# Kernel tuning notes

Measured on AMD Instinct MI355X. Metric: run time of the kernel, lower is better.

Reference implementation:

```python
import jax, jax.numpy as jnp
import numpy as np
import math

# ---- physical constants (QMAV) ----
MASS = 1.5
GRAV = 9.81
_J_NP = np.diag([0.0211, 0.0219, 0.0366]).astype(np.float32)
J = jnp.asarray(_J_NP)
J_INV = jnp.asarray(np.linalg.inv(_J_NP).astype(np.float32))
KD_X = KD_Y = KD_Z = 0.10   # linear drag coeffs
K_H = 0.01                   # horizontal-velocity lift coeff
O_MIN, O_MAX = 0.0, 1000.0   # rotor speed limits [rad/s]
KT, KM, ARM = 1.0e-5, 1.0e-7, 0.15
_G_VEC = jnp.array([0.0, 0.0, GRAV], jnp.float32).reshape(1, 3, 1)  # NED, down positive


def make_G1():
    # [T, Mx, My, Mz] = G_1 @ [o1^2, o2^2, o3^2, o4^2], X-configuration mixer
    c = ARM * KT * math.sqrt(2.0) / 2.0
    return np.array([
        [KT,  KT,  KT,  KT],
        [-c,   c,   c,  -c],
        [-c,  -c,   c,   c],
        [-KM,  KM, -KM,  KM],
    ], dtype=np.float32)


def quat_to_rot(q):
    # q: [B,4,1] = (ew,ex,ey,ez) -> body-to-inertial rotation [B,3,3]
    ew, ex, ey, ez = q[:, 0, 0], q[:, 1, 0], q[:, 2, 0], q[:, 3, 0]
    r = jnp.stack([
        ew**2 + ex**2 - ey**2 - ez**2, 2*(ex*ey - ew*ez), 2*(ex*ez + ew*ey),
        2*(ex*ey + ew*ez), ew**2 - ex**2 + ey**2 - ez**2, 2*(ey*ez - ew*ex),
        2*(ex*ez - ew*ey), 2*(ey*ez + ew*ex), ew**2 - ex**2 - ey**2 + ez**2,
    ], axis=-1)
    return r.reshape(-1, 3, 3)


def quat_to_euler(q):
    ew, ex, ey, ez = q[:, 0:1, :], q[:, 1:2, :], q[:, 2:3, :], q[:, 3:4, :]
    phi = jnp.arctan2(2*(ew*ex + ey*ez), ew**2 + ez**2 - ex**2 - ey**2)
    theta = jnp.arcsin(jnp.clip(2*(ew*ey - ex*ez), -1.0, 1.0))
    psi = jnp.arctan2(2*(ew*ez + ex*ey), ew**2 + ex**2 - ey**2 - ez**2)
    return phi, theta, psi


def rigid_body_deriv(x, u):
    # x: [B,13,1] = [pos(3), v_world(3), quat(4), omega(3)]; u: [B,6,1] = [f_inertial(3), moment_body(3)]
    v = x[:, 3:6, :]
    q = x[:, 6:10, :]
    w = x[:, 10:13, :]
    f_i = u[:, 0:3, :]
    m_b = u[:, 3:6, :]
    pos_dot = v
    v_dot = f_i / MASS + _G_VEC
    ew, ex, ey, ez = q[:, 0:1, :], q[:, 1:2, :], q[:, 2:3, :], q[:, 3:4, :]
    p, qq, r = w[:, 0:1, :], w[:, 1:2, :], w[:, 2:3, :]
    q_dot = 0.5 * jnp.concatenate([
        -ex*p - ey*qq - ez*r,
         ew*p + ey*r - ez*qq,
         ew*qq - ex*r + ez*p,
         ew*r + ex*qq - ey*p,
    ], axis=1)
    Jw = jnp.einsum('ij,bjk->bik', J, w)
    w_dot = jnp.einsum('ij,bjk->bik', J_INV, m_b - jnp.cross(w, Jw, axis=1))
    return jnp.concatenate([pos_dot, v_dot, q_dot, w_dot], axis=1)


def rk4_step(x, u, dt):
    k1 = rigid_body_deriv(x, u)
    k2 = rigid_body_deriv(x + 0.5 * dt * k1, u)
    k3 = rigid_body_deriv(x + 0.5 * dt * k2, u)
    k4 = rigid_body_deriv(x + dt * k3, u)
    return x + (dt / 6.0) * (k1 + 2*k2 + 2*k3 + k4)


def setup_inputs() -> dict:
    key = jax.random.key(0)
    k1, k2 = jax.random.split(key)
    B = 1 << 20
    state = jax.random.normal(k1, (B, 32, 1), dtype=jnp.float32)
    # normalize the quaternion slice so the initial attitude is valid
    q = state[:, 9:13, :]
    state = state.at[:, 9:13, :].set(q / jnp.sqrt(jnp.sum(q**2, axis=1, keepdims=True)))
    delta = jax.random.uniform(k2, (B, 4, 1), dtype=jnp.float32) * O_MAX
    G_1 = jnp.asarray(make_G1())
    return {"state": state, "delta": delta, "G_1": G_1, "dt": 0.02}


def reference(state, delta, G_1, dt):
    # ---- forces / moments + wind-related state ----
    d = jnp.clip(delta, O_MIN, O_MAX)
    tt = jnp.einsum('ij,bjk->bik', G_1, d**2)  # [B,4,1] = [T, Mx, My, Mz]
    T = tt[:, 0:1, :]; Mx = tt[:, 1:2, :]; My = tt[:, 2:3, :]; Mz = tt[:, 3:4, :]
    R = quat_to_rot(state[:, 9:13, :])
    V_wind_b = jnp.einsum('bji,bjk->bik', R, state[:, 28:31, :])  # R^T @ wind_inertial
    u_r = state[:, 16:17, :] - V_wind_b[:, 0:1, :]
    v_r = state[:, 17:18, :] - V_wind_b[:, 1:2, :]
    w_r = state[:, 18:19, :] - V_wind_b[:, 2:3, :]
    Va = jnp.sqrt(u_r**2 + v_r**2 + w_r**2)
    u_safe = jnp.where(u_r == 0.0, 1.0, u_r)
    alpha = jnp.where(u_r == 0.0, math.pi / 2, jnp.arctan2(w_r, u_safe))
    Va_safe = jnp.where(Va == 0.0, 1.0, Va)
    beta = jnp.where(Va == 0.0, 0.0, jnp.arcsin(jnp.clip(v_r / Va_safe, -1.0, 1.0)))
    state = state.at[:, 22:23, :].set(Va)
    state = state.at[:, 24:25, :].set(alpha)
    state = state.at[:, 25:26, :].set(beta)
    fx = -KD_X * u_r
    fy = -KD_Y * v_r
    fz = -T - KD_Z * w_r + K_H * (u_r**2 + v_r**2)
    f_i = R @ jnp.concatenate([fx, fy, fz], axis=1)
    fm = jnp.concatenate([f_i, Mx, My, Mz], axis=1)  # [B,6,1]
    # ---- rigid-body RK4 integration ----
    ode_state = jnp.concatenate(
        [state[:, 3:6, :], state[:, 13:16, :], state[:, 9:13, :], state[:, 19:22, :]], axis=1)
    new = rk4_step(ode_state, fm, dt)
    qn = new[:, 6:10, :]
    qn = qn / jnp.sqrt(jnp.sum(qn**2, axis=1, keepdims=True))
    state = state.at[:, 3:6, :].set(new[:, 0:3, :])
    state = state.at[:, 13:16, :].set(new[:, 3:6, :])
    state = state.at[:, 9:13, :].set(qn)
    state = state.at[:, 19:22, :].set(new[:, 10:13, :])
    # ---- other derived states (R from the pre-update quaternion, as in original) ----
    phi, theta, psi = quat_to_euler(state[:, 9:13, :])
    pdot = R @ state[:, 16:19, :]
    Vg = jnp.sqrt(jnp.sum(pdot**2, axis=(1, 2)))[:, None, None]
    Vg_safe = jnp.where(Vg == 0.0, 1.0, Vg)
    gamma = jnp.arcsin(jnp.clip(pdot[:, 2:3, :] / Vg_safe, -1.0, 1.0))
    chi = jnp.arctan2(pdot[:, 1:2, :], pdot[:, 0:1, :])
    state = state.at[:, 6:7, :].set(phi)
    state = state.at[:, 7:8, :].set(theta)
    state = state.at[:, 8:9, :].set(psi)
    state = state.at[:, 23:24, :].set(Vg)
    state = state.at[:, 26:27, :].set(gamma)
    state = state.at[:, 27:28, :].set(chi)
    return state
```

## Files before the change

kernel.cpp:

```cpp
#include <hip/hip_runtime.h>
#include <math.h>


#define MASSF      1.5f
#define INV_MASSF  (1.0f / 1.5f)
#define GRAVF      9.81f
#define KDF        0.1f
#define KHF        0.01f
#define JXF        0.0211f
#define JYF        0.0219f
#define JZF        0.0366f
#define JIXF       (1.0f / 0.0211f)
#define JIYF       (1.0f / 0.0219f)
#define JIZF       (1.0f / 0.0366f)
#define PI_2F      1.57079632679489661923f

__device__ __forceinline__ void rb_deriv(const float x[13], const float fm[6], float k[13]) {
    k[0] = x[3]; k[1] = x[4]; k[2] = x[5];
    k[3] = fm[0] * INV_MASSF;
    k[4] = fm[1] * INV_MASSF;
    k[5] = fm[2] * INV_MASSF + GRAVF;
    const float ew = x[6], ex = x[7], ey = x[8], ez = x[9];
    const float p = x[10], q = x[11], r = x[12];
    k[6] = 0.5f * (-ex * p - ey * q - ez * r);
    k[7] = 0.5f * ( ew * p + ey * r - ez * q);
    k[8] = 0.5f * ( ew * q - ex * r + ez * p);
    k[9] = 0.5f * ( ew * r + ex * q - ey * p);
    const float Jwx = JXF * p, Jwy = JYF * q, Jwz = JZF * r;
    const float c0 = q * Jwz - r * Jwy;
    const float c1 = r * Jwx - p * Jwz;
    const float c2 = p * Jwy - q * Jwx;
    k[10] = (fm[3] - c0) * JIXF;
    k[11] = (fm[4] - c1) * JIYF;
    k[12] = (fm[5] - c2) * JIZF;
}

__global__ __launch_bounds__(256) void qd_dynamics_kernel(
    const float* __restrict__ state,
    const float* __restrict__ delta,
    const float* __restrict__ G1,
    const float* __restrict__ dtp,
    float* __restrict__ out,
    int B)
{
    const int b = blockIdx.x * blockDim.x + threadIdx.x;
    if (b >= B) return;

    float s[32];
    const float4* sp = (const float4*)(state + (size_t)b * 32);
    float4* sl = (float4*)s;
    #pragma unroll
    for (int i = 0; i < 8; ++i) sl[i] = sp[i];

    const float4 dl = ((const float4*)delta)[b];
    const float dt = dtp[0];

    float g[16];
    const float4* gp = (const float4*)G1;
    float4* gl = (float4*)g;
    #pragma unroll
    for (int i = 0; i < 4; ++i) gl[i] = gp[i];

    float d0 = fminf(fmaxf(dl.x, 0.0f), 1000.0f);
    float d1 = fminf(fmaxf(dl.y, 0.0f), 1000.0f);
    float d2 = fminf(fmaxf(dl.z, 0.0f), 1000.0f);
    float d3 = fminf(fmaxf(dl.w, 0.0f), 1000.0f);
    d0 *= d0; d1 *= d1; d2 *= d2; d3 *= d3;
    const float T  = g[0]  * d0 + g[1]  * d1 + g[2]  * d2 + g[3]  * d3;
    const float Mx = g[4]  * d0 + g[5]  * d1 + g[6]  * d2 + g[7]  * d3;
    const float My = g[8]  * d0 + g[9]  * d1 + g[10] * d2 + g[11] * d3;
    const float Mz = g[12] * d0 + g[13] * d1 + g[14] * d2 + g[15] * d3;

    const float ew = s[9], ex = s[10], ey = s[11], ez = s[12];
    const float r00 = ew*ew + ex*ex - ey*ey - ez*ez;
    const float r01 = 2.0f * (ex*ey - ew*ez);
    const float r02 = 2.0f * (ex*ez + ew*ey);
    const float r10 = 2.0f * (ex*ey + ew*ez);
    const float r11 = ew*ew - ex*ex + ey*ey - ez*ez;
    const float r12 = 2.0f * (ey*ez - ew*ex);
    const float r20 = 2.0f * (ex*ez - ew*ey);
    const float r21 = 2.0f * (ey*ez + ew*ex);
    const float r22 = ew*ew - ex*ex - ey*ey + ez*ez;

    const float wx = s[28], wy = s[29], wz = s[30];
    const float vwb0 = r00 * wx + r10 * wy + r20 * wz;
    const float vwb1 = r01 * wx + r11 * wy + r21 * wz;
    const float vwb2 = r02 * wx + r12 * wy + r22 * wz;

    const float u_r = s[16] - vwb0;
    const float v_r = s[17] - vwb1;
    const float w_r = s[18] - vwb2;
    const float Va = sqrtf(u_r * u_r + v_r * v_r + w_r * w_r);
    const float alpha = (u_r == 0.0f) ? PI_2F : atan2f(w_r, u_r);
    const float beta = (Va == 0.0f)
        ? 0.0f
        : asinf(fminf(fmaxf(v_r / Va, -1.0f), 1.0f));

    const float fx = -KDF * u_r;
    const float fy = -KDF * v_r;
    const float fz = -T - KDF * w_r + KHF * (u_r * u_r + v_r * v_r);
    float fm[6];
    fm[0] = r00 * fx + r01 * fy + r02 * fz;
    fm[1] = r10 * fx + r11 * fy + r12 * fz;
    fm[2] = r20 * fx + r21 * fy + r22 * fz;
    fm[3] = Mx; fm[4] = My; fm[5] = Mz;

    float x0[13];
    x0[0] = s[3];  x0[1] = s[4];  x0[2] = s[5];
    x0[3] = s[13]; x0[4] = s[14]; x0[5] = s[15];
    x0[6] = s[9];  x0[7] = s[10]; x0[8] = s[11]; x0[9] = s[12];
    x0[10] = s[19]; x0[11] = s[20]; x0[12] = s[21];

    float k1[13], k2[13], k3[13], k4[13], xt[13], xn[13];
    rb_deriv(x0, fm, k1);
    #pragma unroll
    for (int i = 0; i < 13; ++i) xt[i] = x0[i] + 0.5f * dt * k1[i];
    rb_deriv(xt, fm, k2);
    #pragma unroll
    for (int i = 0; i < 13; ++i) xt[i] = x0[i] + 0.5f * dt * k2[i];
    rb_deriv(xt, fm, k3);
    #pragma unroll
    for (int i = 0; i < 13; ++i) xt[i] = x0[i] + dt * k3[i];
    rb_deriv(xt, fm, k4);
    const float dt6 = dt / 6.0f;
    #pragma unroll
    for (int i = 0; i < 13; ++i)
        xn[i] = x0[i] + dt6 * (k1[i] + 2.0f * k2[i] + 2.0f * k3[i] + k4[i]);

    float qw = xn[6], qx = xn[7], qy = xn[8], qz = xn[9];
    const float qn = sqrtf(qw * qw + qx * qx + qy * qy + qz * qz);
    qw /= qn; qx /= qn; qy /= qn; qz /= qn;

    const float phi = atan2f(2.0f * (qw * qx + qy * qz),
                             qw * qw + qz * qz - qx * qx - qy * qy);
    const float theta = asinf(fminf(fmaxf(2.0f * (qw * qy - qx * qz), -1.0f), 1.0f));
    const float psi = atan2f(2.0f * (qw * qz + qx * qy),
                             qw * qw + qx * qx - qy * qy - qz * qz);

    const float p0 = r00 * s[16] + r01 * s[17] + r02 * s[18];
    const float p1 = r10 * s[16] + r11 * s[17] + r12 * s[18];
    const float p2 = r20 * s[16] + r21 * s[17] + r22 * s[18];
    const float Vg = sqrtf(p0 * p0 + p1 * p1 + p2 * p2);
    const float vg_safe = (Vg == 0.0f) ? 1.0f : Vg;
    const float gamma = asinf(fminf(fmaxf(p2 / vg_safe, -1.0f), 1.0f));
    const float chi = atan2f(p1, p0);

    float o[32];
    o[0] = s[0]; o[1] = s[1]; o[2] = s[2];
    o[3] = xn[0]; o[4] = xn[1]; o[5] = xn[2];
    o[6] = phi; o[7] = theta; o[8] = psi;
    o[9] = qw; o[10] = qx; o[11] = qy; o[12] = qz;
    o[13] = xn[3]; o[14] = xn[4]; o[15] = xn[5];
    o[16] = s[16]; o[17] = s[17]; o[18] = s[18];
    o[19] = xn[10]; o[20] = xn[11]; o[21] = xn[12];
    o[22] = Va; o[23] = Vg;
    o[24] = alpha; o[25] = beta;
    o[26] = gamma; o[27] = chi;
    o[28] = s[28]; o[29] = s[29]; o[30] = s[30]; o[31] = s[31];

    float4* op = (float4*)(out + (size_t)b * 32);
    const float4* ol = (const float4*)o;
    #pragma unroll
    for (int i = 0; i < 8; ++i) op[i] = ol[i];
}

extern "C" void kernel_launch(void* const* d_in, const int* in_sizes, int n_in,
                              void* d_out, int out_size, void* d_ws, size_t ws_size,
                              hipStream_t stream) {
    const float* state = (const float*)d_in[0];
    const float* delta = (const float*)d_in[1];
    const float* G1    = (const float*)d_in[2];
    const float* dtp   = (const float*)d_in[3];
    float* out = (float*)d_out;
    const int B = in_sizes[0] / 32;
    const int block = 256;
    const int grid = (B + block - 1) / block;
    hipLaunchKernelGGL(qd_dynamics_kernel, dim3(grid), dim3(block), 0, stream,
                       state, delta, G1, dtp, out, B);
}
```

Baseline: 266.5 us.

## Stage state rows through padded LDS for coalesced global loads and stores

Each block now loads its 256 rows of 32-float state with fully coalesced float4 accesses into padded shared memory, then each thread reads its own row from LDS. The output goes back through the same LDS staging before a coalesced write. This targets the strided per-thread 128-byte row accesses of the original. In exchange it adds 36KB of LDS per block, two barriers, and a separate path for the partial tail block.

```diff
diff --git a/kernel.cpp b/kernel.cpp
--- a/kernel.cpp
+++ b/kernel.cpp
@@ -2,7 +2,6 @@
 #include <math.h>
 
 
-#define MASSF      1.5f
 #define INV_MASSF  (1.0f / 1.5f)
 #define GRAVF      9.81f
 #define KDF        0.1f
@@ -14,6 +13,9 @@
 #define JIYF       (1.0f / 0.0219f)
 #define JIZF       (1.0f / 0.0366f)
 #define PI_2F      1.57079632679489661923f
+
+#define ROWS    256
+#define STRIDE  36
 
 __device__ __forceinline__ void rb_deriv(const float x[13], const float fm[6], float k[13]) {
     k[0] = x[3]; k[1] = x[4]; k[2] = x[5];
@@ -35,32 +37,9 @@
     k[12] = (fm[5] - c2) * JIZF;
 }
 
-__global__ __launch_bounds__(256) void qd_dynamics_kernel(
-    const float* __restrict__ state,
-    const float* __restrict__ delta,
-    const float* __restrict__ G1,
-    const float* __restrict__ dtp,
-    float* __restrict__ out,
-    int B)
-{
-    const int b = blockIdx.x * blockDim.x + threadIdx.x;
-    if (b >= B) return;
-
-    float s[32];
-    const float4* sp = (const float4*)(state + (size_t)b * 32);
-    float4* sl = (float4*)s;
-    #pragma unroll
-    for (int i = 0; i < 8; ++i) sl[i] = sp[i];
-
-    const float4 dl = ((const float4*)delta)[b];
-    const float dt = dtp[0];
-
-    float g[16];
-    const float4* gp = (const float4*)G1;
-    float4* gl = (float4*)g;
-    #pragma unroll
-    for (int i = 0; i < 4; ++i) gl[i] = gp[i];
-
+__device__ __forceinline__ void qd_compute(const float s[32], float4 dl,
+                                           const float g[16], float dt,
+                                           float o[32]) {
     float d0 = fminf(fmaxf(dl.x, 0.0f), 1000.0f);
     float d1 = fminf(fmaxf(dl.y, 0.0f), 1000.0f);
     float d2 = fminf(fmaxf(dl.z, 0.0f), 1000.0f);
@@ -145,7 +124,6 @@
     const float gamma = asinf(fminf(fmaxf(p2 / vg_safe, -1.0f), 1.0f));
     const float chi = atan2f(p1, p0);
 
-    float o[32];
     o[0] = s[0]; o[1] = s[1]; o[2] = s[2];
     o[3] = xn[0]; o[4] = xn[1]; o[5] = xn[2];
     o[6] = phi; o[7] = theta; o[8] = psi;
@@ -157,11 +135,84 @@
     o[24] = alpha; o[25] = beta;
     o[26] = gamma; o[27] = chi;
     o[28] = s[28]; o[29] = s[29]; o[30] = s[30]; o[31] = s[31];
-
-    float4* op = (float4*)(out + (size_t)b * 32);
-    const float4* ol = (const float4*)o;
-    #pragma unroll
-    for (int i = 0; i < 8; ++i) op[i] = ol[i];
+}
+
+__global__ __launch_bounds__(ROWS) void qd_dynamics_kernel(
+    const float* __restrict__ state,
+    const float* __restrict__ delta,
+    const float* __restrict__ G1,
+    const float* __restrict__ dtp,
+    float* __restrict__ out,
+    int B)
+{
+    __shared__ float lds[ROWS * STRIDE];
+
+    const int tid = threadIdx.x;
+    const int row0 = blockIdx.x * ROWS;
+    const bool full = (row0 + ROWS) <= B;
+
+    const float dt = dtp[0];
+    float g[16];
+    {
+        const float4* gp = (const float4*)G1;
+        float4* gl = (float4*)g;
+        #pragma unroll
+        for (int i = 0; i < 4; ++i) gl[i] = gp[i];
+    }
+
+    float s[32], o[32];
+    float4 dl;
+
+    if (full) {
+        const float4* gp4 = (const float4*)(state + (size_t)row0 * 32);
+        #pragma unroll
+        for (int i = 0; i < 8; ++i) {
+            const int f4 = i * ROWS + tid;
+            const int f  = f4 * 4;
+            const int r  = f >> 5;
+            const int c  = f & 31;
+            *(float4*)&lds[r * STRIDE + c] = gp4[f4];
+        }
+        __syncthreads();
+        #pragma unroll
+        for (int i = 0; i < 8; ++i)
+            ((float4*)s)[i] = *(const float4*)&lds[tid * STRIDE + i * 4];
+        dl = ((const float4*)delta)[row0 + tid];
+    } else {
+        const int b = row0 + tid;
+        const int bb = (b < B) ? b : (B - 1);
+        const float4* sp = (const float4*)(state + (size_t)bb * 32);
+        #pragma unroll
+        for (int i = 0; i < 8; ++i) ((float4*)s)[i] = sp[i];
+        dl = ((const float4*)delta)[bb];
+        __syncthreads();
+    }
+
+    qd_compute(s, dl, g, dt, o);
+
+    if (full) {
+        #pragma unroll
+        for (int i = 0; i < 8; ++i)
+            *(float4*)&lds[tid * STRIDE + i * 4] = ((const float4*)o)[i];
+        __syncthreads();
+        float4* op4 = (float4*)(out + (size_t)row0 * 32);
+        #pragma unroll
+        for (int i = 0; i < 8; ++i) {
+            const int f4 = i * ROWS + tid;
+            const int f  = f4 * 4;
+            const int r  = f >> 5;
+            const int c  = f & 31;
+            op4[f4] = *(const float4*)&lds[r * STRIDE + c];
+        }
+    } else {
+        __syncthreads();
+        const int b = row0 + tid;
+        if (b < B) {
+            float4* op = (float4*)(out + (size_t)b * 32);
+            #pragma unroll
+            for (int i = 0; i < 8; ++i) op[i] = ((const float4*)o)[i];
+        }
+    }
 }
 
 extern "C" void kernel_launch(void* const* d_in, const int* in_sizes, int n_in,
@@ -173,8 +224,7 @@
     const float* dtp   = (const float*)d_in[3];
     float* out = (float*)d_out;
     const int B = in_sizes[0] / 32;
-    const int block = 256;
-    const int grid = (B + block - 1) / block;
-    hipLaunchKernelGGL(qd_dynamics_kernel, dim3(grid), dim3(block), 0, stream,
+    const int grid = (B + ROWS - 1) / ROWS;
+    hipLaunchKernelGGL(qd_dynamics_kernel, dim3(grid), dim3(ROWS), 0, stream,
                        state, delta, G1, dtp, out, B);
 }
```

New measurement: 247.8 us. 7.0% less time.

## Stage state rows through per-wave LDS transpose for coalesced loads/stores, two rows per thread

Applied to the files above, without the earlier changes.

Each wave now loads 64 consecutive 128-byte state rows with lane-contiguous float4 accesses, transposes them through a per-wave LDS tile with a rotated column index, and writes outputs back through LDS the same way. Each thread processes two rows and the grid is halved. The RK4 stages are also restructured to keep one running accumulator instead of four k arrays, which reduces register pressure. The costs are 32 KB of LDS per block and extra LDS round trips. The hand-written waitcnt fences also stand in for barriers, which is only valid because each tile is private to one wave.

```diff
diff --git a/kernel.cpp b/kernel.cpp
--- a/kernel.cpp
+++ b/kernel.cpp
@@ -2,7 +2,6 @@
 #include <math.h>
 
 
-#define MASSF      1.5f
 #define INV_MASSF  (1.0f / 1.5f)
 #define GRAVF      9.81f
 #define KDF        0.1f
@@ -14,6 +13,8 @@
 #define JIYF       (1.0f / 0.0219f)
 #define JIZF       (1.0f / 0.0366f)
 #define PI_2F      1.57079632679489661923f
+
+#define FENCE_LDS() __asm__ volatile("s_waitcnt lgkmcnt(0)" ::: "memory")
 
 __device__ __forceinline__ void rb_deriv(const float x[13], const float fm[6], float k[13]) {
     k[0] = x[3]; k[1] = x[4]; k[2] = x[5];
@@ -27,40 +28,14 @@
     k[8] = 0.5f * ( ew * q - ex * r + ez * p);
     k[9] = 0.5f * ( ew * r + ex * q - ey * p);
     const float Jwx = JXF * p, Jwy = JYF * q, Jwz = JZF * r;
-    const float c0 = q * Jwz - r * Jwy;
-    const float c1 = r * Jwx - p * Jwz;
-    const float c2 = p * Jwy - q * Jwx;
-    k[10] = (fm[3] - c0) * JIXF;
-    k[11] = (fm[4] - c1) * JIYF;
-    k[12] = (fm[5] - c2) * JIZF;
-}
-
-__global__ __launch_bounds__(256) void qd_dynamics_kernel(
-    const float* __restrict__ state,
-    const float* __restrict__ delta,
-    const float* __restrict__ G1,
-    const float* __restrict__ dtp,
-    float* __restrict__ out,
-    int B)
-{
-    const int b = blockIdx.x * blockDim.x + threadIdx.x;
-    if (b >= B) return;
-
-    float s[32];
-    const float4* sp = (const float4*)(state + (size_t)b * 32);
-    float4* sl = (float4*)s;
-    #pragma unroll
-    for (int i = 0; i < 8; ++i) sl[i] = sp[i];
-
-    const float4 dl = ((const float4*)delta)[b];
-    const float dt = dtp[0];
-
-    float g[16];
-    const float4* gp = (const float4*)G1;
-    float4* gl = (float4*)g;
-    #pragma unroll
-    for (int i = 0; i < 4; ++i) gl[i] = gp[i];
-
+    k[10] = (fm[3] - (q * Jwz - r * Jwy)) * JIXF;
+    k[11] = (fm[4] - (r * Jwx - p * Jwz)) * JIYF;
+    k[12] = (fm[5] - (p * Jwy - q * Jwx)) * JIZF;
+}
+
+__device__ __forceinline__ void qd_compute(const float s[32], float4 dl,
+                                           const float g[16], float dt,
+                                           float o[32]) {
     float d0 = fminf(fmaxf(dl.x, 0.0f), 1000.0f);
     float d1 = fminf(fmaxf(dl.y, 0.0f), 1000.0f);
     float d2 = fminf(fmaxf(dl.z, 0.0f), 1000.0f);
@@ -111,21 +86,21 @@
     x0[6] = s[9];  x0[7] = s[10]; x0[8] = s[11]; x0[9] = s[12];
     x0[10] = s[19]; x0[11] = s[20]; x0[12] = s[21];
 
-    float k1[13], k2[13], k3[13], k4[13], xt[13], xn[13];
-    rb_deriv(x0, fm, k1);
-    #pragma unroll
-    for (int i = 0; i < 13; ++i) xt[i] = x0[i] + 0.5f * dt * k1[i];
-    rb_deriv(xt, fm, k2);
-    #pragma unroll
-    for (int i = 0; i < 13; ++i) xt[i] = x0[i] + 0.5f * dt * k2[i];
-    rb_deriv(xt, fm, k3);
-    #pragma unroll
-    for (int i = 0; i < 13; ++i) xt[i] = x0[i] + dt * k3[i];
-    rb_deriv(xt, fm, k4);
+    const float hdt = 0.5f * dt;
     const float dt6 = dt / 6.0f;
-    #pragma unroll
-    for (int i = 0; i < 13; ++i)
-        xn[i] = x0[i] + dt6 * (k1[i] + 2.0f * k2[i] + 2.0f * k3[i] + k4[i]);
+    float k[13], acc[13], xt[13], xn[13];
+    rb_deriv(x0, fm, k);
+    #pragma unroll
+    for (int i = 0; i < 13; ++i) { acc[i] = k[i]; xt[i] = x0[i] + hdt * k[i]; }
+    rb_deriv(xt, fm, k);
+    #pragma unroll
+    for (int i = 0; i < 13; ++i) { acc[i] += 2.0f * k[i]; xt[i] = x0[i] + hdt * k[i]; }
+    rb_deriv(xt, fm, k);
+    #pragma unroll
+    for (int i = 0; i < 13; ++i) { acc[i] += 2.0f * k[i]; xt[i] = x0[i] + dt * k[i]; }
+    rb_deriv(xt, fm, k);
+    #pragma unroll
+    for (int i = 0; i < 13; ++i) xn[i] = x0[i] + dt6 * (acc[i] + k[i]);
 
     float qw = xn[6], qx = xn[7], qy = xn[8], qz = xn[9];
     const float qn = sqrtf(qw * qw + qx * qx + qy * qy + qz * qz);
@@ -145,7 +120,6 @@
     const float gamma = asinf(fminf(fmaxf(p2 / vg_safe, -1.0f), 1.0f));
     const float chi = atan2f(p1, p0);
 
-    float o[32];
     o[0] = s[0]; o[1] = s[1]; o[2] = s[2];
     o[3] = xn[0]; o[4] = xn[1]; o[5] = xn[2];
     o[6] = phi; o[7] = theta; o[8] = psi;
@@ -157,11 +131,120 @@
     o[24] = alpha; o[25] = beta;
     o[26] = gamma; o[27] = chi;
     o[28] = s[28]; o[29] = s[29]; o[30] = s[30]; o[31] = s[31];
-
-    float4* op = (float4*)(out + (size_t)b * 32);
-    const float4* ol = (const float4*)o;
-    #pragma unroll
-    for (int i = 0; i < 8; ++i) op[i] = ol[i];
+}
+
+__global__ __launch_bounds__(256) void qd_dynamics_kernel(
+    const float* __restrict__ state,
+    const float* __restrict__ delta,
+    const float* __restrict__ G1,
+    const float* __restrict__ dtp,
+    float* __restrict__ out,
+    int B)
+{
+    __shared__ float lds[4][64 * 32];
+
+    const int tid  = threadIdx.x;
+    const int lane = tid & 63;
+    const int wave = tid >> 6;
+    float* tile = &lds[wave][0];
+
+    const int rowA = blockIdx.x * 512 + wave * 128;
+    const int rowB = rowA + 64;
+
+    const float dt = dtp[0];
+    float g[16];
+    {
+        const float4* gp = (const float4*)G1;
+        #pragma unroll
+        for (int i = 0; i < 4; ++i) ((float4*)g)[i] = gp[i];
+    }
+
+    float sA[32], sB[32], o[32];
+
+    if (rowB + 64 <= B) {
+        const float4* gA4 = (const float4*)(state + (size_t)rowA * 32);
+        const float4* gB4 = (const float4*)(state + (size_t)rowB * 32);
+        float4 gA[8], gB[8];
+        #pragma unroll
+        for (int i = 0; i < 8; ++i) gA[i] = gA4[i * 64 + lane];
+        #pragma unroll
+        for (int i = 0; i < 8; ++i) gB[i] = gB4[i * 64 + lane];
+        const float4 dlA = ((const float4*)delta)[rowA + lane];
+        const float4 dlB = ((const float4*)delta)[rowB + lane];
+
+        #pragma unroll
+        for (int i = 0; i < 8; ++i) {
+            const int f4 = i * 64 + lane;
+            *(float4*)&tile[(f4 >> 3) * 32 + (f4 & 7) * 4] = gA[i];
+        }
+        FENCE_LDS();
+        #pragma unroll
+        for (int i = 0; i < 8; ++i) {
+            const int c = (i + lane) & 7;
+            ((float4*)sA)[c] = *(const float4*)&tile[lane * 32 + c * 4];
+        }
+        FENCE_LDS();
+        #pragma unroll
+        for (int i = 0; i < 8; ++i) {
+            const int f4 = i * 64 + lane;
+            *(float4*)&tile[(f4 >> 3) * 32 + (f4 & 7) * 4] = gB[i];
+        }
+        FENCE_LDS();
+        #pragma unroll
+        for (int i = 0; i < 8; ++i) {
+            const int c = (i + lane) & 7;
+            ((float4*)sB)[c] = *(const float4*)&tile[lane * 32 + c * 4];
+        }
+
+        qd_compute(sA, dlA, g, dt, o);
+        FENCE_LDS();
+        #pragma unroll
+        for (int j = 0; j < 8; ++j) {
+            const int c = (j + lane) & 7;
+            *(float4*)&tile[lane * 32 + c * 4] = ((const float4*)o)[c];
+        }
+        FENCE_LDS();
+        {
+            float4* oA4 = (float4*)(out + (size_t)rowA * 32);
+            #pragma unroll
+            for (int i = 0; i < 8; ++i) {
+                const int f4 = i * 64 + lane;
+                oA4[f4] = *(const float4*)&tile[(f4 >> 3) * 32 + (f4 & 7) * 4];
+            }
+        }
+        FENCE_LDS();
+
+        qd_compute(sB, dlB, g, dt, o);
+        #pragma unroll
+        for (int j = 0; j < 8; ++j) {
+            const int c = (j + lane) & 7;
+            *(float4*)&tile[lane * 32 + c * 4] = ((const float4*)o)[c];
+        }
+        FENCE_LDS();
+        {
+            float4* oB4 = (float4*)(out + (size_t)rowB * 32);
+            #pragma unroll
+            for (int i = 0; i < 8; ++i) {
+                const int f4 = i * 64 + lane;
+                oB4[f4] = *(const float4*)&tile[(f4 >> 3) * 32 + (f4 & 7) * 4];
+            }
+        }
+    } else {
+        #pragma unroll
+        for (int u = 0; u < 2; ++u) {
+            const int b = rowA + u * 64 + lane;
+            if (b < B) {
+                const float4* sp = (const float4*)(state + (size_t)b * 32);
+                #pragma unroll
+                for (int i = 0; i < 8; ++i) ((float4*)sA)[i] = sp[i];
+                const float4 dl = ((const float4*)delta)[b];
+                qd_compute(sA, dl, g, dt, o);
+                float4* op = (float4*)(out + (size_t)b * 32);
+                #pragma unroll
+                for (int i = 0; i < 8; ++i) op[i] = ((const float4*)o)[i];
+            }
+        }
+    }
 }
 
 extern "C" void kernel_launch(void* const* d_in, const int* in_sizes, int n_in,
@@ -173,8 +256,7 @@
     const float* dtp   = (const float*)d_in[3];
     float* out = (float*)d_out;
     const int B = in_sizes[0] / 32;
-    const int block = 256;
-    const int grid = (B + block - 1) / block;
-    hipLaunchKernelGGL(qd_dynamics_kernel, dim3(grid), dim3(block), 0, stream,
+    const int grid = (B + 511) / 512;
+    hipLaunchKernelGGL(qd_dynamics_kernel, dim3(grid), dim3(256), 0, stream,
                        state, delta, G1, dtp, out, B);
 }
```

Measured after the change: 409.4 us. 1.54x slower.
